# Kernel tuning notes

Hardware: AMD Instinct MI355X
Metric: run time of the kernel (lower is better)

The kernel has to match this reference:

```python
import jax, jax.numpy as jnp
import numpy as np

D_MODEL = 1024
NUM_HEADS = 16
D_K = D_MODEL // NUM_HEADS


def setup_inputs() -> dict:
    key = jax.random.key(0)
    ks = jax.random.split(key, 6)
    B, S = 2, 2048
    scale = 1.0 / np.sqrt(D_MODEL)
    x = jax.random.normal(ks[0], (B, S, D_MODEL), dtype=jnp.float32)
    w_q = jax.random.normal(ks[1], (D_MODEL, D_MODEL), dtype=jnp.float32) * scale
    w_k = jax.random.normal(ks[2], (D_MODEL, D_MODEL), dtype=jnp.float32) * scale
    w_v = jax.random.normal(ks[3], (D_MODEL, D_MODEL), dtype=jnp.float32) * scale
    w_o = jax.random.normal(ks[4], (D_MODEL, D_MODEL), dtype=jnp.float32) * scale
    b_o = jax.random.normal(ks[5], (D_MODEL,), dtype=jnp.float32) * 0.01
    return {"x": x, "w_q": w_q, "w_k": w_k, "w_v": w_v, "w_o": w_o, "b_o": b_o}


def reference(x, w_q, w_k, w_v, w_o, b_o):
    B, S, _ = x.shape
    # Linear(d, d, bias=False): y = x @ W.T ; weights stored torch-style [out, in]
    def proj(w):
        y = jnp.einsum('bsd,ed->bse', x, w)
        return y.reshape(B, S, NUM_HEADS, D_K).transpose(0, 2, 1, 3)  # [B,H,S,Dk]
    Q, K, V = proj(w_q), proj(w_k), proj(w_v)
    scores = jnp.einsum('bhqd,bhkd->bhqk', Q, K) / np.sqrt(D_K)
    attn = jax.nn.softmax(scores, axis=-1)  # dropout p=0 (eval) -> identity
    out = jnp.einsum('bhqk,bhkd->bhqd', attn, V)
    out = out.transpose(0, 2, 1, 3).reshape(B, S, D_MODEL)
    return jnp.einsum('bsd,ed->bse', out, w_o) + b_o
```

## Files before the change

kernel.cpp:

```cpp
#include <hip/hip_runtime.h>
#include <hip/hip_bf16.h>


typedef __bf16 bf16x8 __attribute__((ext_vector_type(8)));
typedef float f32x4 __attribute__((ext_vector_type(4)));

__device__ __forceinline__ unsigned short f2bf(float f) {
  union { float f; unsigned int u; } c; c.f = f;
  unsigned int u = c.u;
  return (unsigned short)((u + 0x7FFFu + ((u >> 16) & 1u)) >> 16);
}

__device__ __forceinline__ unsigned int pk2bf(float a, float b) {
  union { float f; unsigned int u; } x, y;
  x.f = a; y.f = b;
  return __builtin_amdgcn_perm(y.u + 0x8000u, x.u + 0x8000u, 0x07060302u);
}

__device__ __forceinline__ bf16x8 ld_frag(const unsigned short* p) {
  union { uint4 u; bf16x8 b; } c;
  c.u = *(const uint4*)p;
  return c.b;
}

__device__ __forceinline__ uint4 cvt8(const float* __restrict__ p) {
  float4 a = *(const float4*)p;
  float4 b = *(const float4*)(p + 4);
  union { uint4 u; unsigned short s[8]; } r;
  r.s[0] = f2bf(a.x); r.s[1] = f2bf(a.y); r.s[2] = f2bf(a.z); r.s[3] = f2bf(a.w);
  r.s[4] = f2bf(b.x); r.s[5] = f2bf(b.y); r.s[6] = f2bf(b.z); r.s[7] = f2bf(b.w);
  return r.u;
}

typedef __attribute__((address_space(1))) const unsigned int as1_u32;
typedef __attribute__((address_space(3))) unsigned int as3_u32;
__device__ __forceinline__ void async16(const unsigned short* g,
                                        unsigned short* l) {
  __builtin_amdgcn_global_load_lds(
      (as1_u32*)(unsigned long long)g,
      (as3_u32*)(unsigned int)(unsigned long long)l, 16, 0, 0);
}

__global__ __launch_bounds__(256) void cvt_all(
    const float* __restrict__ s0, const float* __restrict__ s1,
    const float* __restrict__ s2, const float* __restrict__ s3,
    const float* __restrict__ s4,
    unsigned short* __restrict__ d0, unsigned short* __restrict__ d1,
    unsigned short* __restrict__ d2, unsigned short* __restrict__ d3,
    unsigned short* __restrict__ d4) {
  const float* srcs[5] = {s0, s1, s2, s3, s4};
  unsigned short* dsts[5] = {d0, d1, d2, d3, d4};
  const int ns[5] = {4194304, 1048576, 1048576, 1048576, 1048576};
  const int y = blockIdx.y;
  const int idx = (blockIdx.x * 256 + threadIdx.x) * 8;
  if (idx >= ns[y]) return;
  *(uint4*)(dsts[y] + idx) = cvt8(srcs[y] + idx);
}

template <int BM, bool OUT_F32>
__global__ __launch_bounds__(256) void gemm_bt(
    const unsigned short* __restrict__ A,
    const unsigned short* __restrict__ w0,
    const unsigned short* __restrict__ w1,
    const unsigned short* __restrict__ w2,
    const float* __restrict__ bias,
    void* __restrict__ outraw, float z0scale) {
  constexpr int NT = (BM == 128) ? 4 : 2;
  const int z = blockIdx.z;
  const unsigned short* W = (z == 0) ? w0 : ((z == 1) ? w1 : w2);
  const float scl = (z == 0) ? z0scale : 1.0f;

  __shared__ unsigned short a_lds[BM * 32];
  __shared__ unsigned short b_lds[128 * 32];

  const int tid = threadIdx.x;
  const int wave = tid >> 6, lane = tid & 63;
  const int quad = lane >> 4, l16 = lane & 15;
  const int wm = (BM == 128) ? (wave >> 1) * 64 : 0;
  const int wn = (BM == 128) ? (wave & 1) * 64 : wave * 32;
  const int bm = blockIdx.y * BM, bn = blockIdx.x * 128;

  const int rl = lane >> 2;
  const int kc = (lane & 3) ^ (rl & 3) ^ ((rl >> 2) & 3);
  const int arow = (BM == 128) ? (wave * 32 + rl) : (wave * 16 + rl);
  const unsigned short* ga = A + (size_t)(bm + arow) * 1024 + kc * 8;
  const unsigned short* gb = W + (size_t)(bn + wave * 32 + rl) * 1024 + kc * 8;
  unsigned short* la = &a_lds[arow - rl + 0] + 0;
  la = &a_lds[((BM == 128) ? wave * 32 : wave * 16) * 32];
  unsigned short* lb = &b_lds[wave * 32 * 32];

  const int rsw8 = ((l16 & 3) ^ ((l16 >> 2) & 3)) * 8;

  f32x4 acc[4][NT] = {};

  for (int k0 = 0; k0 < 1024; k0 += 32) {
    async16(ga, la);
    if (BM == 128) async16(ga + 16 * 1024, la + 16 * 32);
    async16(gb, lb);
    async16(gb + 16 * 1024, lb + 16 * 32);
    ga += 32; gb += 32;
    __syncthreads();

    bf16x8 af[4], bfr[NT];
#pragma unroll
    for (int t = 0; t < 4; ++t)
      af[t] = ld_frag(&a_lds[(wm + t * 16 + l16) * 32 + ((quad * 8) ^ rsw8)]);
#pragma unroll
    for (int t = 0; t < NT; ++t)
      bfr[t] = ld_frag(&b_lds[(wn + t * 16 + l16) * 32 + ((quad * 8) ^ rsw8)]);
#pragma unroll
    for (int mt = 0; mt < 4; ++mt)
#pragma unroll
      for (int nt = 0; nt < NT; ++nt)
        acc[mt][nt] = __builtin_amdgcn_mfma_f32_16x16x32_bf16(
            af[mt], bfr[nt], acc[mt][nt], 0, 0, 0);
    __syncthreads();
  }

#pragma unroll
  for (int nt = 0; nt < NT; ++nt) {
    const int n = bn + wn + nt * 16 + l16;
    const float bv = bias ? bias[n] : 0.0f;
#pragma unroll
    for (int mt = 0; mt < 4; ++mt)
#pragma unroll
      for (int r = 0; r < 4; ++r) {
        const int m = bm + wm + mt * 16 + quad * 4 + r;
        const float v = acc[mt][nt][r] * scl + bv;
        if (OUT_F32)
          ((float*)outraw)[(size_t)z * 4096 * 1024 + (size_t)m * 1024 + n] = v;
        else
          ((unsigned short*)outraw)[(size_t)z * 4096 * 1024 +
                                    (size_t)m * 1024 + n] = f2bf(v);
      }
  }
}

__global__ __launch_bounds__(256) void transpose_v(
    const unsigned short* __restrict__ v, unsigned short* __restrict__ vt) {
  const int st0 = blockIdx.x * 64;
  const int bh = blockIdx.y, b = bh >> 4, h = bh & 15;
  __shared__ unsigned short t[64 * 72];
  const int tid = threadIdx.x;
#pragma unroll
  for (int it = 0; it < 2; ++it) {
    const int c = it * 256 + tid;
    const int row = c >> 3, c8 = (c & 7) * 8;
    *(uint4*)&t[row * 72 + c8] =
        *(const uint4*)(v + (size_t)(b * 2048 + st0 + row) * 1024 + h * 64 + c8);
  }
  __syncthreads();
#pragma unroll
  for (int it = 0; it < 2; ++it) {
    const int c = it * 256 + tid;
    const int drow = c >> 3, s8 = (c & 7) * 8;
    union { uint4 u; unsigned short e[8]; } o;
#pragma unroll
    for (int j = 0; j < 8; ++j) o.e[j] = t[(s8 + j) * 72 + drow];
    *(uint4*)(vt + ((size_t)bh * 64 + drow) * 2048 + st0 + s8) = o.u;
  }
}

__global__ __launch_bounds__(256) void attn3(
    const unsigned short* __restrict__ qkv,
    const unsigned short* __restrict__ vt_g,
    unsigned short* __restrict__ ab) {
  constexpr size_t PL = (size_t)4096 * 1024;
  const int qt = blockIdx.x, bh = blockIdx.y;
  const int b = bh >> 4, h = bh & 15;

  __shared__ unsigned short kp[128 * 136];
  __shared__ unsigned short vtl[64 * 136];

  const int tid = threadIdx.x;
  const int wave = tid >> 6, lane = tid & 63;
  const int quad = lane >> 4, l16 = lane & 15;
  const int qb = quad * 20;

  const unsigned short* Kp = qkv + PL + ((size_t)b * 2048) * 1024 + h * 64;
  const unsigned short* Vt = vt_g + (size_t)bh * 64 * 2048;

  bf16x8 qf[2][2];
#pragma unroll
  for (int hf = 0; hf < 2; ++hf) {
    const unsigned short* qrow =
        qkv + (size_t)(b * 2048 + qt * 128 + wave * 32 + hf * 16 + l16) * 1024 +
        h * 64;
    union { uint4 u; bf16x8 bv; } c;
    c.u = *(const uint4*)(qrow + quad * 8);       qf[hf][0] = c.bv;
    c.u = *(const uint4*)(qrow + 32 + quad * 8);  qf[hf][1] = c.bv;
  }

  f32x4 o_acc[2][4] = {};
  float l_part[2] = {0.0f, 0.0f};

  for (int kv0 = 0; kv0 < 2048; kv0 += 128) {
    __syncthreads();
#pragma unroll
    for (int it = 0; it < 4; ++it) {
      const int c = it * 256 + tid;
      const int kr = c >> 3, kc = (c & 7) * 8;
      *(uint4*)&kp[kr * 72 + kc] =
          *(const uint4*)(Kp + (size_t)(kv0 + kr) * 1024 + kc);
      const int vr = c >> 4, vc = (c & 15) * 8;
      *(uint4*)&vtl[vr * 136 + vc] =
          *(const uint4*)(Vt + (size_t)vr * 2048 + kv0 + vc);
    }
    __syncthreads();

    f32x4 st[2][8] = {};
#pragma unroll
    for (int mb = 0; mb < 8; ++mb) {
      bf16x8 ak0 = ld_frag(&kp[(mb * 16 + l16) * 72 + quad * 8]);
      bf16x8 ak1 = ld_frag(&kp[(mb * 16 + l16) * 72 + 32 + quad * 8]);
#pragma unroll
      for (int hf = 0; hf < 2; ++hf) {
        st[hf][mb] = __builtin_amdgcn_mfma_f32_16x16x32_bf16(
            ak0, qf[hf][0], st[hf][mb], 0, 0, 0);
        st[hf][mb] = __builtin_amdgcn_mfma_f32_16x16x32_bf16(
            ak1, qf[hf][1], st[hf][mb], 0, 0, 0);
      }
    }

#pragma unroll
    for (int hf = 0; hf < 2; ++hf)
#pragma unroll
      for (int mb = 0; mb < 8; ++mb)
#pragma unroll
        for (int r = 0; r < 4; ++r) {
          const float p = __builtin_amdgcn_exp2f(st[hf][mb][r]);
          st[hf][mb][r] = p;
          l_part[hf] += p;
        }

    __syncthreads();
#pragma unroll
    for (int hf = 0; hf < 2; ++hf)
#pragma unroll
      for (int mb = 0; mb < 8; ++mb) {
        uint2 pk;
        pk.x = pk2bf(st[hf][mb][0], st[hf][mb][1]);
        pk.y = pk2bf(st[hf][mb][2], st[hf][mb][3]);
        *(uint2*)&kp[(wave * 32 + hf * 16 + l16) * 136 + mb * 16 + quad * 4] =
            pk;
      }

#pragma unroll
    for (int ks = 0; ks < 4; ++ks) {
      bf16x8 bvf[4];
#pragma unroll
      for (int nt = 0; nt < 4; ++nt)
        bvf[nt] = ld_frag(&vtl[(nt * 16 + l16) * 136 + ks * 32 + quad * 8]);
#pragma unroll
      for (int hf = 0; hf < 2; ++hf) {
        bf16x8 ap =
            ld_frag(&kp[(wave * 32 + hf * 16 + l16) * 136 + ks * 32 + quad * 8]);
#pragma unroll
        for (int nt = 0; nt < 4; ++nt)
          o_acc[hf][nt] = __builtin_amdgcn_mfma_f32_16x16x32_bf16(
              ap, bvf[nt], o_acc[hf][nt], 0, 0, 0);
      }
    }
  }

#pragma unroll
  for (int hf = 0; hf < 2; ++hf) {
    float lp = l_part[hf];
    lp += __shfl_xor(lp, 16);
    lp += __shfl_xor(lp, 32);
    float lr[4];
#pragma unroll
    for (int r = 0; r < 4; ++r) lr[r] = 1.0f / __shfl(lp, qb + r);
#pragma unroll
    for (int nt = 0; nt < 4; ++nt)
#pragma unroll
      for (int r = 0; r < 4; ++r) {
        const int row = qt * 128 + wave * 32 + hf * 16 + quad * 4 + r;
        ab[((size_t)b * 2048 + row) * 1024 + h * 64 + nt * 16 + l16] =
            f2bf(o_acc[hf][nt][r] * lr[r]);
      }
  }
}

extern "C" void kernel_launch(void* const* d_in, const int* in_sizes, int n_in,
                              void* d_out, int out_size, void* d_ws,
                              size_t ws_size, hipStream_t stream) {
  const float* x  = (const float*)d_in[0];
  const float* wq = (const float*)d_in[1];
  const float* wk = (const float*)d_in[2];
  const float* wv = (const float*)d_in[3];
  const float* wo = (const float*)d_in[4];
  const float* bo = (const float*)d_in[5];

  constexpr size_t PL = (size_t)4096 * 1024;
  unsigned short* qkv = (unsigned short*)d_ws;
  unsigned short* ab  = qkv + 2 * PL;
  unsigned short* xb  = qkv + 3 * PL;
  unsigned short* vt  = xb;
  unsigned short* wqb = qkv + 4 * PL;
  unsigned short* wkb = wqb + 1024 * 1024;
  unsigned short* wvb = wkb + 1024 * 1024;
  unsigned short* wob = wvb + 1024 * 1024;

  const float QSCALE = 0.18033688011112042f;

  cvt_all<<<dim3(2048, 5), 256, 0, stream>>>(x, wq, wk, wv, wo,
                                             xb, wqb, wkb, wvb, wob);
  gemm_bt<128, false><<<dim3(8, 32, 3), 256, 0, stream>>>(
      xb, wqb, wkb, wvb, nullptr, qkv, QSCALE);
  transpose_v<<<dim3(32, 32), 256, 0, stream>>>(qkv + 2 * PL, vt);
  attn3<<<dim3(16, 32), 256, 0, stream>>>(qkv, vt, ab);
  gemm_bt<64, true><<<dim3(8, 64, 1), 256, 0, stream>>>(
      ab, wob, wob, wob, bo, d_out, 1.0f);
}
```

Before: 222.1 us.

## Load K and V fragments directly from global memory, use per-wave P buffers

The attention kernel stops staging K and V tiles through shared memory. Each wave now loads its MFMA operand fragments for K and V straight from global memory into registers, and the probability tile goes into a private per-wave LDS buffer. This removes all block-wide __syncthreads in the KV loop. In exchange, the four waves of a block each re-read the same K/V data from global memory/L2 instead of sharing one copy, and the kernel uses more registers to hold the K fragments.

Result: slower. 261.1 us (+17.6%).

```diff
diff --git a/kernel.cpp b/kernel.cpp
--- a/kernel.cpp
+++ b/kernel.cpp
@@ -18,6 +18,12 @@
 }
 
 __device__ __forceinline__ bf16x8 ld_frag(const unsigned short* p) {
+  union { uint4 u; bf16x8 b; } c;
+  c.u = *(const uint4*)p;
+  return c.b;
+}
+
+__device__ __forceinline__ bf16x8 gld_frag(const unsigned short* p) {
   union { uint4 u; bf16x8 b; } c;
   c.u = *(const uint4*)p;
   return c.b;
@@ -85,8 +91,7 @@
   const int arow = (BM == 128) ? (wave * 32 + rl) : (wave * 16 + rl);
   const unsigned short* ga = A + (size_t)(bm + arow) * 1024 + kc * 8;
   const unsigned short* gb = W + (size_t)(bn + wave * 32 + rl) * 1024 + kc * 8;
-  unsigned short* la = &a_lds[arow - rl + 0] + 0;
-  la = &a_lds[((BM == 128) ? wave * 32 : wave * 16) * 32];
+  unsigned short* la = &a_lds[((BM == 128) ? wave * 32 : wave * 16) * 32];
   unsigned short* lb = &b_lds[wave * 32 * 32];
 
   const int rsw8 = ((l16 & 3) ^ ((l16 >> 2) & 3)) * 8;
@@ -161,7 +166,7 @@
   }
 }
 
-__global__ __launch_bounds__(256) void attn3(
+__global__ __launch_bounds__(256) void attn4(
     const unsigned short* __restrict__ qkv,
     const unsigned short* __restrict__ vt_g,
     unsigned short* __restrict__ ab) {
@@ -169,13 +174,13 @@
   const int qt = blockIdx.x, bh = blockIdx.y;
   const int b = bh >> 4, h = bh & 15;
 
-  __shared__ unsigned short kp[128 * 136];
-  __shared__ unsigned short vtl[64 * 136];
+  __shared__ unsigned short P[4][32 * 136];
 
   const int tid = threadIdx.x;
   const int wave = tid >> 6, lane = tid & 63;
   const int quad = lane >> 4, l16 = lane & 15;
   const int qb = quad * 20;
+  unsigned short* Pw = P[wave];
 
   const unsigned short* Kp = qkv + PL + ((size_t)b * 2048) * 1024 + h * 64;
   const unsigned short* Vt = vt_g + (size_t)bh * 64 * 2048;
@@ -191,74 +196,66 @@
     c.u = *(const uint4*)(qrow + 32 + quad * 8);  qf[hf][1] = c.bv;
   }
 
+  const unsigned short* kbase = Kp + (size_t)l16 * 1024 + quad * 8;
+  const unsigned short* vbase = Vt + (size_t)l16 * 2048 + quad * 8;
+
   f32x4 o_acc[2][4] = {};
   float l_part[2] = {0.0f, 0.0f};
 
   for (int kv0 = 0; kv0 < 2048; kv0 += 128) {
-    __syncthreads();
-#pragma unroll
-    for (int it = 0; it < 4; ++it) {
-      const int c = it * 256 + tid;
-      const int kr = c >> 3, kc = (c & 7) * 8;
-      *(uint4*)&kp[kr * 72 + kc] =
-          *(const uint4*)(Kp + (size_t)(kv0 + kr) * 1024 + kc);
-      const int vr = c >> 4, vc = (c & 15) * 8;
-      *(uint4*)&vtl[vr * 136 + vc] =
-          *(const uint4*)(Vt + (size_t)vr * 2048 + kv0 + vc);
-    }
-    __syncthreads();
+    uint4 kf[8][2];
+#pragma unroll
+    for (int mb = 0; mb < 8; ++mb)
+#pragma unroll
+      for (int ks = 0; ks < 2; ++ks)
+        kf[mb][ks] =
+            *(const uint4*)(kbase + (size_t)(kv0 + mb * 16) * 1024 + ks * 32);
 
     f32x4 st[2][8] = {};
 #pragma unroll
     for (int mb = 0; mb < 8; ++mb) {
-      bf16x8 ak0 = ld_frag(&kp[(mb * 16 + l16) * 72 + quad * 8]);
-      bf16x8 ak1 = ld_frag(&kp[(mb * 16 + l16) * 72 + 32 + quad * 8]);
+      union { uint4 u; bf16x8 bv; } a0, a1;
+      a0.u = kf[mb][0]; a1.u = kf[mb][1];
 #pragma unroll
       for (int hf = 0; hf < 2; ++hf) {
         st[hf][mb] = __builtin_amdgcn_mfma_f32_16x16x32_bf16(
-            ak0, qf[hf][0], st[hf][mb], 0, 0, 0);
+            a0.bv, qf[hf][0], st[hf][mb], 0, 0, 0);
         st[hf][mb] = __builtin_amdgcn_mfma_f32_16x16x32_bf16(
-            ak1, qf[hf][1], st[hf][mb], 0, 0, 0);
+            a1.bv, qf[hf][1], st[hf][mb], 0, 0, 0);
       }
     }
 
 #pragma unroll
     for (int hf = 0; hf < 2; ++hf)
 #pragma unroll
-      for (int mb = 0; mb < 8; ++mb)
+      for (int mb = 0; mb < 8; ++mb) {
 #pragma unroll
         for (int r = 0; r < 4; ++r) {
           const float p = __builtin_amdgcn_exp2f(st[hf][mb][r]);
           st[hf][mb][r] = p;
           l_part[hf] += p;
         }
-
-    __syncthreads();
-#pragma unroll
-    for (int hf = 0; hf < 2; ++hf)
-#pragma unroll
-      for (int mb = 0; mb < 8; ++mb) {
         uint2 pk;
         pk.x = pk2bf(st[hf][mb][0], st[hf][mb][1]);
         pk.y = pk2bf(st[hf][mb][2], st[hf][mb][3]);
-        *(uint2*)&kp[(wave * 32 + hf * 16 + l16) * 136 + mb * 16 + quad * 4] =
-            pk;
-      }
-
-#pragma unroll
-    for (int ks = 0; ks < 4; ++ks) {
+        *(uint2*)&Pw[(hf * 16 + l16) * 136 + mb * 16 + quad * 4] = pk;
+      }
+
+#pragma unroll
+    for (int ks2 = 0; ks2 < 4; ++ks2) {
       bf16x8 bvf[4];
 #pragma unroll
       for (int nt = 0; nt < 4; ++nt)
-        bvf[nt] = ld_frag(&vtl[(nt * 16 + l16) * 136 + ks * 32 + quad * 8]);
-#pragma unroll
-      for (int hf = 0; hf < 2; ++hf) {
-        bf16x8 ap =
-            ld_frag(&kp[(wave * 32 + hf * 16 + l16) * 136 + ks * 32 + quad * 8]);
-#pragma unroll
-        for (int nt = 0; nt < 4; ++nt)
-          o_acc[hf][nt] = __builtin_amdgcn_mfma_f32_16x16x32_bf16(
-              ap, bvf[nt], o_acc[hf][nt], 0, 0, 0);
+        bvf[nt] =
+            gld_frag(vbase + (size_t)(nt * 16) * 2048 + kv0 + ks2 * 32);
+      bf16x8 ap0 = ld_frag(&Pw[l16 * 136 + ks2 * 32 + quad * 8]);
+      bf16x8 ap1 = ld_frag(&Pw[(16 + l16) * 136 + ks2 * 32 + quad * 8]);
+#pragma unroll
+      for (int nt = 0; nt < 4; ++nt) {
+        o_acc[0][nt] = __builtin_amdgcn_mfma_f32_16x16x32_bf16(
+            ap0, bvf[nt], o_acc[0][nt], 0, 0, 0);
+        o_acc[1][nt] = __builtin_amdgcn_mfma_f32_16x16x32_bf16(
+            ap1, bvf[nt], o_acc[1][nt], 0, 0, 0);
       }
     }
   }
@@ -309,7 +306,7 @@
   gemm_bt<128, false><<<dim3(8, 32, 3), 256, 0, stream>>>(
       xb, wqb, wkb, wvb, nullptr, qkv, QSCALE);
   transpose_v<<<dim3(32, 32), 256, 0, stream>>>(qkv + 2 * PL, vt);
-  attn3<<<dim3(16, 32), 256, 0, stream>>>(qkv, vt, ab);
+  attn4<<<dim3(16, 32), 256, 0, stream>>>(qkv, vt, ab);
   gemm_bt<64, true><<<dim3(8, 64, 1), 256, 0, stream>>>(
       ab, wob, wob, wob, bo, d_out, 1.0f);
 }
```

## Register-prefetch next K/V tile and give each wave a private P buffer

Applied to the files above, without the earlier changes.

The attention kernel now loads the next K and V^T tile into registers while the current tile is being computed, then writes those registers to LDS at the top of the next iteration. This hides global-memory latency behind the MFMA work. P now goes to a separate LDS buffer per wave instead of reusing the K buffer, which removes the mid-iteration __syncthreads. The cost is more LDS (about 69KB in total), which can lower occupancy, and extra registers for the prefetch.

Measured after the change: 240.8 us. 1.08x slower.

```diff
diff --git a/kernel.cpp b/kernel.cpp
--- a/kernel.cpp
+++ b/kernel.cpp
@@ -85,8 +85,7 @@
   const int arow = (BM == 128) ? (wave * 32 + rl) : (wave * 16 + rl);
   const unsigned short* ga = A + (size_t)(bm + arow) * 1024 + kc * 8;
   const unsigned short* gb = W + (size_t)(bn + wave * 32 + rl) * 1024 + kc * 8;
-  unsigned short* la = &a_lds[arow - rl + 0] + 0;
-  la = &a_lds[((BM == 128) ? wave * 32 : wave * 16) * 32];
+  unsigned short* la = &a_lds[((BM == 128) ? wave * 32 : wave * 16) * 32];
   unsigned short* lb = &b_lds[wave * 32 * 32];
 
   const int rsw8 = ((l16 & 3) ^ ((l16 >> 2) & 3)) * 8;
@@ -161,7 +160,7 @@
   }
 }
 
-__global__ __launch_bounds__(256) void attn3(
+__global__ __launch_bounds__(256) void attn5(
     const unsigned short* __restrict__ qkv,
     const unsigned short* __restrict__ vt_g,
     unsigned short* __restrict__ ab) {
@@ -169,13 +168,15 @@
   const int qt = blockIdx.x, bh = blockIdx.y;
   const int b = bh >> 4, h = bh & 15;
 
-  __shared__ unsigned short kp[128 * 136];
+  __shared__ unsigned short kl[128 * 72];
   __shared__ unsigned short vtl[64 * 136];
+  __shared__ unsigned short pl[4][32 * 136];
 
   const int tid = threadIdx.x;
   const int wave = tid >> 6, lane = tid & 63;
   const int quad = lane >> 4, l16 = lane & 15;
   const int qb = quad * 20;
+  unsigned short* Pw = pl[wave];
 
   const unsigned short* Kp = qkv + PL + ((size_t)b * 2048) * 1024 + h * 64;
   const unsigned short* Vt = vt_g + (size_t)bh * 64 * 2048;
@@ -191,6 +192,14 @@
     c.u = *(const uint4*)(qrow + 32 + quad * 8);  qf[hf][1] = c.bv;
   }
 
+  uint4 kreg[4], vreg[4];
+#pragma unroll
+  for (int it = 0; it < 4; ++it) {
+    const int c = it * 256 + tid;
+    kreg[it] = *(const uint4*)(Kp + (size_t)(c >> 3) * 1024 + (c & 7) * 8);
+    vreg[it] = *(const uint4*)(Vt + (size_t)(c >> 4) * 2048 + (c & 15) * 8);
+  }
+
   f32x4 o_acc[2][4] = {};
   float l_part[2] = {0.0f, 0.0f};
 
@@ -199,20 +208,28 @@
 #pragma unroll
     for (int it = 0; it < 4; ++it) {
       const int c = it * 256 + tid;
-      const int kr = c >> 3, kc = (c & 7) * 8;
-      *(uint4*)&kp[kr * 72 + kc] =
-          *(const uint4*)(Kp + (size_t)(kv0 + kr) * 1024 + kc);
-      const int vr = c >> 4, vc = (c & 15) * 8;
-      *(uint4*)&vtl[vr * 136 + vc] =
-          *(const uint4*)(Vt + (size_t)vr * 2048 + kv0 + vc);
+      *(uint4*)&kl[(c >> 3) * 72 + (c & 7) * 8] = kreg[it];
+      *(uint4*)&vtl[(c >> 4) * 136 + (c & 15) * 8] = vreg[it];
     }
     __syncthreads();
 
+    if (kv0 + 128 < 2048) {
+      const int nkv = kv0 + 128;
+#pragma unroll
+      for (int it = 0; it < 4; ++it) {
+        const int c = it * 256 + tid;
+        kreg[it] =
+            *(const uint4*)(Kp + (size_t)(nkv + (c >> 3)) * 1024 + (c & 7) * 8);
+        vreg[it] =
+            *(const uint4*)(Vt + (size_t)(c >> 4) * 2048 + nkv + (c & 15) * 8);
+      }
+    }
+
     f32x4 st[2][8] = {};
 #pragma unroll
     for (int mb = 0; mb < 8; ++mb) {
-      bf16x8 ak0 = ld_frag(&kp[(mb * 16 + l16) * 72 + quad * 8]);
-      bf16x8 ak1 = ld_frag(&kp[(mb * 16 + l16) * 72 + 32 + quad * 8]);
+      bf16x8 ak0 = ld_frag(&kl[(mb * 16 + l16) * 72 + quad * 8]);
+      bf16x8 ak1 = ld_frag(&kl[(mb * 16 + l16) * 72 + 32 + quad * 8]);
 #pragma unroll
       for (int hf = 0; hf < 2; ++hf) {
         st[hf][mb] = __builtin_amdgcn_mfma_f32_16x16x32_bf16(
@@ -225,24 +242,17 @@
 #pragma unroll
     for (int hf = 0; hf < 2; ++hf)
 #pragma unroll
-      for (int mb = 0; mb < 8; ++mb)
+      for (int mb = 0; mb < 8; ++mb) {
 #pragma unroll
         for (int r = 0; r < 4; ++r) {
           const float p = __builtin_amdgcn_exp2f(st[hf][mb][r]);
           st[hf][mb][r] = p;
           l_part[hf] += p;
         }
-
-    __syncthreads();
-#pragma unroll
-    for (int hf = 0; hf < 2; ++hf)
-#pragma unroll
-      for (int mb = 0; mb < 8; ++mb) {
         uint2 pk;
         pk.x = pk2bf(st[hf][mb][0], st[hf][mb][1]);
         pk.y = pk2bf(st[hf][mb][2], st[hf][mb][3]);
-        *(uint2*)&kp[(wave * 32 + hf * 16 + l16) * 136 + mb * 16 + quad * 4] =
-            pk;
+        *(uint2*)&Pw[(hf * 16 + l16) * 136 + mb * 16 + quad * 4] = pk;
       }
 
 #pragma unroll
@@ -253,8 +263,7 @@
         bvf[nt] = ld_frag(&vtl[(nt * 16 + l16) * 136 + ks * 32 + quad * 8]);
 #pragma unroll
       for (int hf = 0; hf < 2; ++hf) {
-        bf16x8 ap =
-            ld_frag(&kp[(wave * 32 + hf * 16 + l16) * 136 + ks * 32 + quad * 8]);
+        bf16x8 ap = ld_frag(&Pw[(hf * 16 + l16) * 136 + ks * 32 + quad * 8]);
 #pragma unroll
         for (int nt = 0; nt < 4; ++nt)
           o_acc[hf][nt] = __builtin_amdgcn_mfma_f32_16x16x32_bf16(
@@ -309,7 +318,7 @@
   gemm_bt<128, false><<<dim3(8, 32, 3), 256, 0, stream>>>(
       xb, wqb, wkb, wvb, nullptr, qkv, QSCALE);
   transpose_v<<<dim3(32, 32), 256, 0, stream>>>(qkv + 2 * PL, vt);
-  attn3<<<dim3(16, 32), 256, 0, stream>>>(qkv, vt, ab);
+  attn5<<<dim3(16, 32), 256, 0, stream>>>(qkv, vt, ab);
   gemm_bt<64, true><<<dim3(8, 64, 1), 256, 0, stream>>>(
       ab, wob, wob, wob, bo, d_out, 1.0f);
 }
```

## Split attention over two KV halves and add a combine kernel

Applied to the files above, without the earlier changes.

The attention kernel now splits the 2048-long KV range into two halves across a third grid dimension, doubling the block count. Each half writes unnormalized bf16 partial outputs and per-row exp-sum partials to workspace. A new combine kernel sums the two partials and divides by the total sum. This targets under-filled CUs from the previous 512-block grid, at the cost of an extra launch, extra global traffic for the partial buffers, and one more bf16 rounding of unnormalized values.

Result: slower. 229.8 us (+3.5%).

```diff
diff --git a/kernel.cpp b/kernel.cpp
--- a/kernel.cpp
+++ b/kernel.cpp
@@ -9,6 +9,11 @@
   union { float f; unsigned int u; } c; c.f = f;
   unsigned int u = c.u;
   return (unsigned short)((u + 0x7FFFu + ((u >> 16) & 1u)) >> 16);
+}
+
+__device__ __forceinline__ float b2f(unsigned short u) {
+  union { unsigned int u; float f; } c; c.u = ((unsigned int)u) << 16;
+  return c.f;
 }
 
 __device__ __forceinline__ unsigned int pk2bf(float a, float b) {
@@ -85,8 +90,7 @@
   const int arow = (BM == 128) ? (wave * 32 + rl) : (wave * 16 + rl);
   const unsigned short* ga = A + (size_t)(bm + arow) * 1024 + kc * 8;
   const unsigned short* gb = W + (size_t)(bn + wave * 32 + rl) * 1024 + kc * 8;
-  unsigned short* la = &a_lds[arow - rl + 0] + 0;
-  la = &a_lds[((BM == 128) ? wave * 32 : wave * 16) * 32];
+  unsigned short* la = &a_lds[((BM == 128) ? wave * 32 : wave * 16) * 32];
   unsigned short* lb = &b_lds[wave * 32 * 32];
 
   const int rsw8 = ((l16 & 3) ^ ((l16 >> 2) & 3)) * 8;
@@ -161,13 +165,15 @@
   }
 }
 
-__global__ __launch_bounds__(256) void attn3(
+__global__ __launch_bounds__(256) void attn6(
     const unsigned short* __restrict__ qkv,
     const unsigned short* __restrict__ vt_g,
-    unsigned short* __restrict__ ab) {
+    unsigned short* __restrict__ opart,
+    float* __restrict__ lpart) {
   constexpr size_t PL = (size_t)4096 * 1024;
-  const int qt = blockIdx.x, bh = blockIdx.y;
+  const int qt = blockIdx.x, bh = blockIdx.y, kvh = blockIdx.z;
   const int b = bh >> 4, h = bh & 15;
+  const int kvbase = kvh * 1024;
 
   __shared__ unsigned short kp[128 * 136];
   __shared__ unsigned short vtl[64 * 136];
@@ -175,10 +181,10 @@
   const int tid = threadIdx.x;
   const int wave = tid >> 6, lane = tid & 63;
   const int quad = lane >> 4, l16 = lane & 15;
-  const int qb = quad * 20;
-
-  const unsigned short* Kp = qkv + PL + ((size_t)b * 2048) * 1024 + h * 64;
-  const unsigned short* Vt = vt_g + (size_t)bh * 64 * 2048;
+
+  const unsigned short* Kp =
+      qkv + PL + ((size_t)b * 2048 + kvbase) * 1024 + h * 64;
+  const unsigned short* Vt = vt_g + (size_t)bh * 64 * 2048 + kvbase;
 
   bf16x8 qf[2][2];
 #pragma unroll
@@ -194,7 +200,7 @@
   f32x4 o_acc[2][4] = {};
   float l_part[2] = {0.0f, 0.0f};
 
-  for (int kv0 = 0; kv0 < 2048; kv0 += 128) {
+  for (int kv0 = 0; kv0 < 1024; kv0 += 128) {
     __syncthreads();
 #pragma unroll
     for (int it = 0; it < 4; ++it) {
@@ -263,23 +269,48 @@
     }
   }
 
+  unsigned short* Op = opart + (size_t)kvh * PL;
 #pragma unroll
   for (int hf = 0; hf < 2; ++hf) {
     float lp = l_part[hf];
     lp += __shfl_xor(lp, 16);
     lp += __shfl_xor(lp, 32);
-    float lr[4];
-#pragma unroll
-    for (int r = 0; r < 4; ++r) lr[r] = 1.0f / __shfl(lp, qb + r);
+    const int q = qt * 128 + wave * 32 + hf * 16 + l16;
+    if (quad == 0)
+      lpart[((size_t)kvh * 32 + bh) * 2048 + q] = lp;
 #pragma unroll
     for (int nt = 0; nt < 4; ++nt)
 #pragma unroll
       for (int r = 0; r < 4; ++r) {
         const int row = qt * 128 + wave * 32 + hf * 16 + quad * 4 + r;
-        ab[((size_t)b * 2048 + row) * 1024 + h * 64 + nt * 16 + l16] =
-            f2bf(o_acc[hf][nt][r] * lr[r]);
-      }
-  }
+        Op[((size_t)b * 2048 + row) * 1024 + h * 64 + nt * 16 + l16] =
+            f2bf(o_acc[hf][nt][r]);
+      }
+  }
+}
+
+__global__ __launch_bounds__(256) void attn_combine(
+    const unsigned short* __restrict__ opart,
+    const float* __restrict__ lpart,
+    unsigned short* __restrict__ ab) {
+  constexpr size_t PL = (size_t)4096 * 1024;
+  const int gid = blockIdx.x * 256 + threadIdx.x;
+  const int s = gid >> 7;
+  const int c = (gid & 127) * 8;
+  const int b = s >> 11, q = s & 2047, h = c >> 6;
+  const size_t li = (size_t)(b * 16 + h) * 2048 + q;
+  const float inv = 1.0f / (lpart[li] + lpart[32 * 2048 + li]);
+  const size_t off = (size_t)s * 1024 + c;
+  union { uint4 u; unsigned short e[8]; } a, bv, o;
+  a.u = *(const uint4*)(opart + off);
+  bv.u = *(const uint4*)(opart + PL + off);
+#pragma unroll
+  for (int j = 0; j < 8; j += 2) {
+    const float v0 = (b2f(a.e[j]) + b2f(bv.e[j])) * inv;
+    const float v1 = (b2f(a.e[j + 1]) + b2f(bv.e[j + 1])) * inv;
+    *(unsigned int*)&o.e[j] = pk2bf(v0, v1);
+  }
+  *(uint4*)(ab + off) = o.u;
 }
 
 extern "C" void kernel_launch(void* const* d_in, const int* in_sizes, int n_in,
@@ -301,6 +332,8 @@
   unsigned short* wkb = wqb + 1024 * 1024;
   unsigned short* wvb = wkb + 1024 * 1024;
   unsigned short* wob = wvb + 1024 * 1024;
+  unsigned short* opart = wob + 1024 * 1024;
+  float* lpart = (float*)(opart + 2 * PL);
 
   const float QSCALE = 0.18033688011112042f;
 
@@ -309,7 +342,8 @@
   gemm_bt<128, false><<<dim3(8, 32, 3), 256, 0, stream>>>(
       xb, wqb, wkb, wvb, nullptr, qkv, QSCALE);
   transpose_v<<<dim3(32, 32), 256, 0, stream>>>(qkv + 2 * PL, vt);
-  attn3<<<dim3(16, 32), 256, 0, stream>>>(qkv, vt, ab);
+  attn6<<<dim3(16, 32, 2), 256, 0, stream>>>(qkv, vt, opart, lpart);
+  attn_combine<<<dim3(2048), 256, 0, stream>>>(opart, lpart, ab);
   gemm_bt<64, true><<<dim3(8, 64, 1), 256, 0, stream>>>(
       ab, wob, wob, wob, bo, d_out, 1.0f);
 }
```
